# Performance work log

Hardware: AMD Instinct MI355X
Metric: run time of the kernel (lower is better)

The kernel has to match this reference:

```python
import jax, jax.numpy as jnp
import numpy as np
from jax import lax

NPOINTS = [1024, 256, 64, 16]
RADII = [0.02, 0.04, 0.06, 0.08]
NSAMPLE = [32, 32, 16, 16]
# per-level MLP widths; first entry already includes the +3 for use_xyz concat
MLPS = [[6, 32, 32, 64], [67, 64, 64, 128], [131, 128, 128, 256], [259, 256, 256, 512]]
EPS = 1e-5


def setup_inputs() -> dict:
    key = jax.random.key(0)
    B, N = 8, 16384
    pc = jax.random.uniform(jax.random.fold_in(key, 0), (B, N, 6), jnp.float32)
    # xyz into a 0.2-cube so the hard-coded radii (0.02..0.08) find real neighborhoods
    pc = pc.at[..., :3].multiply(0.2)
    inp = {"pointcloud": pc}
    ki = 1
    for l, m in enumerate(MLPS):
        for j in range(len(m) - 1):
            cin, cout = m[j], m[j + 1]
            inp[f"w{l}{j}"] = jax.random.normal(jax.random.fold_in(key, ki), (cin, cout), jnp.float32) * (1.0 / float(np.sqrt(cin)))
            inp[f"g{l}{j}"] = jnp.ones((cout,), jnp.float32)
            inp[f"b{l}{j}"] = jnp.zeros((cout,), jnp.float32)
            ki += 1
    return inp


def _fps(xyz, npoint):
    # iterative farthest point sampling, start at index 0 (matches CUDA kernel)
    B, N, _ = xyz.shape

    def step(carry, _):
        mind, last = carry
        lastp = jnp.take_along_axis(xyz, last[:, None, None], axis=1)  # [B,1,3]
        d = jnp.sum((xyz - lastp) ** 2, axis=-1)                       # [B,N]
        mind = jnp.minimum(mind, d)
        nxt = jnp.argmax(mind, axis=1).astype(jnp.int32)
        return (mind, nxt), last

    init = (jnp.full((B, N), 1e10, xyz.dtype), jnp.zeros((B,), jnp.int32))
    _, idx = lax.scan(step, init, None, length=npoint)
    return jnp.transpose(idx)  # [B,npoint]


def _gather(pts, idx):
    # pts [B,N,C], idx [B,...] -> [B,...,C]
    return jax.vmap(lambda p, i: p[i])(pts, idx)


def _ball_query(xyz, centers, radius, nsample):
    # first nsample points (in index order) within radius; pad with first hit (0 if none)
    N = xyz.shape[1]
    d2 = jnp.sum((centers[:, :, None, :] - xyz[:, None, :, :]) ** 2, axis=-1)  # [B,S,N]
    key = jnp.where(d2 < radius * radius, jnp.arange(N, dtype=jnp.int32), N)
    negtop, _ = lax.top_k(-key, nsample)
    sel = -negtop                      # ascending candidate indices
    valid = sel < N
    first = jnp.where(valid[..., :1], sel[..., :1], 0)
    return jnp.where(valid, sel, first)  # [B,S,nsample] int32


def _sa(xyz, feats, npoint, radius, nsample, layers):
    fps_idx = lax.stop_gradient(_fps(xyz, npoint))
    new_xyz = _gather(xyz, fps_idx)                    # [B,S,3]
    idx = _ball_query(xyz, new_xyz, radius, nsample)   # [B,S,K]
    g = _gather(xyz, idx) - new_xyz[:, :, None, :]     # centered grouped xyz [B,S,K,3]
    g = jnp.concatenate([g, _gather(feats, idx)], axis=-1)  # use_xyz concat -> [B,S,K,3+C]
    x = g
    for W, gamma, beta in layers:
        x = jnp.einsum('bski,io->bsko', x, W)          # 1x1 conv, bias=False (bn on)
        mu = jnp.mean(x, axis=(0, 1, 2))               # BN training-mode batch stats
        var = jnp.var(x, axis=(0, 1, 2))
        x = jax.nn.relu(gamma * (x - mu) * lax.rsqrt(var + EPS) + beta)
    return new_xyz, jnp.max(x, axis=2)                 # max-pool over neighbors -> [B,S,Cout]


def reference(pointcloud, w00, g00, b00, w01, g01, b01, w02, g02, b02,
              w10, g10, b10, w11, g11, b11, w12, g12, b12,
              w20, g20, b20, w21, g21, b21, w22, g22, b22,
              w30, g30, b30, w31, g31, b31, w32, g32, b32):
    params = [
        [(w00, g00, b00), (w01, g01, b01), (w02, g02, b02)],
        [(w10, g10, b10), (w11, g11, b11), (w12, g12, b12)],
        [(w20, g20, b20), (w21, g21, b21), (w22, g22, b22)],
        [(w30, g30, b30), (w31, g31, b31), (w32, g32, b32)],
    ]
    xyz = pointcloud[..., :3]
    feats = pointcloud[..., 3:]   # channels-last (torch keeps [B,C,N]; pure layout diff)
    l_xyz, l_feats = [xyz], [feats]
    for k in range(4):
        nx, nf = _sa(l_xyz[k], l_feats[k], NPOINTS[k], RADII[k], NSAMPLE[k], params[k])
        l_xyz.append(nx)
        l_feats.append(nf)
    return tuple(l_xyz) + tuple(l_feats)
```

## Files before the change

kernel.cpp:

```cpp
#include <hip/hip_runtime.h>

#define WAVE 64

__global__ __launch_bounds__(256) void split_kernel(const float* __restrict__ pc,
    float* __restrict__ xyz, float* __restrict__ feats, int total) {
  int t = blockIdx.x * blockDim.x + threadIdx.x;
  if (t >= total) return;
  const float* p = pc + (size_t)t * 6;
  xyz[t * 3 + 0] = p[0]; xyz[t * 3 + 1] = p[1]; xyz[t * 3 + 2] = p[2];
  feats[t * 3 + 0] = p[3]; feats[t * 3 + 1] = p[4]; feats[t * 3 + 2] = p[5];
}

__global__ __launch_bounds__(256) void zero_kernel(float* __restrict__ p, int n) {
  int t = blockIdx.x * blockDim.x + threadIdx.x;
  if (t < n) p[t] = 0.f;
}

__device__ __forceinline__ unsigned mapf(float f) {
  unsigned b = __float_as_uint(f);
  return (b & 0x80000000u) ? ~b : (b | 0x80000000u);
}
__device__ __forceinline__ float unmapf(unsigned u) {
  unsigned b = (u & 0x80000000u) ? (u ^ 0x80000000u) : ~u;
  return __uint_as_float(b);
}

__device__ __forceinline__ unsigned long long dpp_max_u64(unsigned long long v) {
#define DPP_STEP_U64(ctrl) { \
    unsigned lo_ = (unsigned)v, hi_ = (unsigned)(v >> 32); \
    unsigned tlo_ = (unsigned)__builtin_amdgcn_update_dpp((int)lo_, (int)lo_, ctrl, 0xf, 0xf, false); \
    unsigned thi_ = (unsigned)__builtin_amdgcn_update_dpp((int)hi_, (int)hi_, ctrl, 0xf, 0xf, false); \
    unsigned long long t_ = ((unsigned long long)thi_ << 32) | tlo_; \
    if (t_ > v) v = t_; }
  DPP_STEP_U64(0x111) DPP_STEP_U64(0x112) DPP_STEP_U64(0x114)
  DPP_STEP_U64(0x118) DPP_STEP_U64(0x142) DPP_STEP_U64(0x143)
#undef DPP_STEP_U64
  return v;
}

#define FPS_W   8
#define FPS_PT  8
__global__ __launch_bounds__(256, 4) void fps_big_multi_kernel(
    const float* __restrict__ xyz, float* __restrict__ new_xyz,
    unsigned long long* __restrict__ gkey, int N, int S) {
  const int b = blockIdx.x & 7;
  const int w = blockIdx.x >> 3;
  const int tid = threadIdx.x;
  const int lane = tid & 63;
  const int wv = tid >> 6;
  const float* px = xyz + (size_t)b * N * 3;
  const int base = w * (FPS_PT * 256);
  __shared__ unsigned long long s_cand[4];
  __shared__ unsigned long long s_win;
  float rx[FPS_PT], ry[FPS_PT], rz[FPS_PT], mind[FPS_PT];
#pragma unroll
  for (int p = 0; p < FPS_PT; ++p) {
    int i = base + p * 256 + tid;
    rx[p] = px[i * 3 + 0]; ry[p] = px[i * 3 + 1]; rz[p] = px[i * 3 + 2];
    asm volatile("" : "+v"(rx[p]), "+v"(ry[p]), "+v"(rz[p]));
    mind[p] = 1e10f;
  }
  float qx = px[0], qy = px[1], qz = px[2];
  if (w == 0 && tid == 0) {
    float* o = new_xyz + (size_t)b * S * 3;
    o[0] = qx; o[1] = qy; o[2] = qz;
  }
  unsigned long long* slots = gkey + (size_t)b * S * FPS_W;
  for (unsigned it = 1; it < (unsigned)S; ++it) {
    float bestv = -1.f; unsigned besti = 0;
#pragma unroll
    for (int p = 0; p < FPS_PT; ++p) {
      float dx = __fsub_rn(rx[p], qx);
      float dy = __fsub_rn(ry[p], qy);
      float dz = __fsub_rn(rz[p], qz);
      float d = __fadd_rn(__fadd_rn(__fmul_rn(dx, dx), __fmul_rn(dy, dy)), __fmul_rn(dz, dz));
      float mo = fminf(mind[p], d);
      mind[p] = mo;
      if (mo > bestv) { bestv = mo; besti = (unsigned)(base + p * 256 + tid); }
    }
    unsigned long long key = ((unsigned long long)__float_as_uint(bestv) << 32)
                           | (0xFFFFFFFFu - besti);
    key = dpp_max_u64(key);
    if (lane == 63) s_cand[wv] = key;
    __syncthreads();
    if (tid < 64) {
      unsigned long long k = s_cand[lane & 3];
#pragma unroll
      for (int off = 1; off < 4; off <<= 1) {
        unsigned long long o = __shfl_xor(k, off, 4);
        if (o > k) k = o;
      }
      if (lane == 0) {
        atomicExch(&slots[(size_t)it * FPS_W + w], k);
      }
      unsigned long long kk = 0ull;
      if (lane < FPS_W) {
        unsigned long long* sl = &slots[(size_t)it * FPS_W + lane];
        unsigned long long t0 = __builtin_amdgcn_s_memrealtime();
        int r = 0;
        for (;;) {
          kk = __hip_atomic_load(sl, __ATOMIC_RELAXED, __HIP_MEMORY_SCOPE_AGENT);
          if (kk) break;
          if (++r > 256) {
            kk = atomicMax(sl, 0ull);
            if (kk) break;
            if (__builtin_amdgcn_s_memrealtime() - t0 > 2000000ull) {
              kk = 0xFFFFFFFFull;
              break;
            }
            __builtin_amdgcn_s_sleep(1);
          }
        }
      }
#pragma unroll
      for (int off = 1; off < FPS_W; off <<= 1) {
        unsigned long long o = __shfl_xor(kk, off, FPS_W);
        if (o > kk) kk = o;
      }
      if (lane == 0) s_win = kk;
    }
    __syncthreads();
    unsigned long long k = s_win;
    int last = (int)((0xFFFFFFFFu - (unsigned)k) & 16383u);
    const float* q = px + (size_t)last * 3;
    qx = q[0]; qy = q[1]; qz = q[2];
    if (w == 0 && tid == 0) {
      float* o = new_xyz + ((size_t)b * S + it) * 3;
      o[0] = qx; o[1] = qy; o[2] = qz;
    }
  }
}

__global__ void fps_small_kernel(const float* __restrict__ xyz,
    float* __restrict__ new_xyz, int N, int S) {
  const int b = blockIdx.x;
  const int tid = threadIdx.x;
  const int lane = tid & 63;
  const int wv = tid >> 6;
  const int NW = N >> 6;
  const float* px = xyz + (size_t)b * N * 3;
  __shared__ float sx[1024], sy[1024], sz[1024];
  __shared__ unsigned long long s_cand[2][16];
  float x = px[tid * 3 + 0], y = px[tid * 3 + 1], z = px[tid * 3 + 2];
  sx[tid] = x; sy[tid] = y; sz[tid] = z;
  float mind = 1e10f;
  float qx = px[0], qy = px[1], qz = px[2];
  if (tid == 0) {
    float* o = new_xyz + (size_t)b * S * 3;
    o[0] = qx; o[1] = qy; o[2] = qz;
  }
  __syncthreads();
  for (unsigned it = 1; it < (unsigned)S; ++it) {
    float dx = __fsub_rn(x, qx);
    float dy = __fsub_rn(y, qy);
    float dz = __fsub_rn(z, qz);
    float d = __fadd_rn(__fadd_rn(__fmul_rn(dx, dx), __fmul_rn(dy, dy)), __fmul_rn(dz, dz));
    mind = fminf(mind, d);
    unsigned long long key = ((unsigned long long)__float_as_uint(mind) << 32)
                           | (0xFFFFFFFFu - (unsigned)tid);
    key = dpp_max_u64(key);
    if (lane == 63) s_cand[it & 1u][wv] = key;
    __syncthreads();
    unsigned long long k = (lane < NW) ? s_cand[it & 1u][lane] : 0ull;
    k = dpp_max_u64(k);
    unsigned klo = (unsigned)__builtin_amdgcn_readlane((int)(unsigned)k, 63);
    int last = (int)(0xFFFFFFFFu - klo);
    qx = sx[last]; qy = sy[last]; qz = sz[last];
    if (tid == 0) {
      float* o = new_xyz + ((size_t)b * S + it) * 3;
      o[0] = qx; o[1] = qy; o[2] = qz;
    }
  }
}

__global__ __launch_bounds__(256) void ballquery_kernel(const float* __restrict__ xyz,
    const float* __restrict__ centers, int* __restrict__ out_idx,
    int N, int S, int nsample, float r2) {
  int gw = (blockIdx.x * blockDim.x + threadIdx.x) >> 6;
  int lane = threadIdx.x & 63;
  int b = gw / S;
  int s = gw - b * S;
  const float* px = xyz + (size_t)b * N * 3;
  const float* cp = centers + ((size_t)b * S + s) * 3;
  float cx = cp[0], cy = cp[1], cz = cp[2];
  int* out = out_idx + ((size_t)b * S + s) * nsample;
  int cnt = 0;
  int firsti = 0;
  for (int base = 0; base < N; base += WAVE) {
    int i = base + lane;
    float dx = __fsub_rn(cx, px[i * 3 + 0]);
    float dy = __fsub_rn(cy, px[i * 3 + 1]);
    float dz = __fsub_rn(cz, px[i * 3 + 2]);
    float d = __fadd_rn(__fadd_rn(__fmul_rn(dx, dx), __fmul_rn(dy, dy)), __fmul_rn(dz, dz));
    bool hit = d < r2;
    unsigned long long m = __ballot(hit);
    if (hit) {
      int slot = cnt + __popcll(m & ((1ull << lane) - 1ull));
      if (slot < nsample) out[slot] = i;
    }
    if (cnt == 0 && m) firsti = base + __ffsll((unsigned long long)m) - 1;
    cnt += __popcll(m);
    if (cnt >= nsample) break;
  }
  for (int q = cnt + lane; q < nsample; q += WAVE) out[q] = firsti;
}

#define BM 64
#define BN 64
#define BK 16
__global__ __launch_bounds__(256) void mm_fused_kernel(const float* __restrict__ A,
    const float* __restrict__ W, float* __restrict__ Y,
    float* __restrict__ st_out, const float* __restrict__ st_in,
    const float* __restrict__ g_in, const float* __restrict__ b_in,
    int R, int C, int Co, float inv_n,
    const int* __restrict__ idx, const float* __restrict__ xyz,
    const float* __restrict__ feats, const float* __restrict__ centers,
    int N, int kshift, int sshift, int ci,
    unsigned* __restrict__ extmax, unsigned* __restrict__ extmin) {
  __shared__ float As[BK][BM + 4];
  __shared__ float Bs[BK][BN + 4];
  __shared__ float s_mu[260], s_rs[260], s_g[260], s_b[260];
  __shared__ float s_sum[BN], s_sq[BN];
  __shared__ int s_idx[BM];
  __shared__ unsigned s_mx[4][BN], s_mn[4][BN];
  int r0 = blockIdx.x * BM;
  int n0 = blockIdx.y * BN;
  int tid = threadIdx.x;
  int tx = tid & 15, ty = tid >> 4;
  if (st_in) {
    for (int c = tid; c < C; c += 256) {
      float mu = st_in[c] * inv_n;
      float var = st_in[512 + c] * inv_n - mu * mu;
      s_mu[c] = mu; s_rs[c] = rsqrtf(var + 1e-5f);
      s_g[c] = g_in[c]; s_b[c] = b_in[c];
    }
  }
  if (idx && tid < BM) s_idx[tid] = idx[r0 + tid];
  if (tid < BN) { s_sum[tid] = 0.f; s_sq[tid] = 0.f; }
  if (extmax) {
    for (int t2 = tid; t2 < 4 * BN; t2 += 256) {
      ((unsigned*)s_mx)[t2] = 0u;
      ((unsigned*)s_mn)[t2] = 0xFFFFFFFFu;
    }
  }
  __syncthreads();
  float acc[4][4] = {};
  for (int k0 = 0; k0 < C; k0 += BK) {
#pragma unroll
    for (int u = 0; u < 4; ++u) {
      int lin = tid + u * 256;
      int row = lin >> 4;
      int cc = lin & 15;
      int c = k0 + cc;
      float v = 0.f;
      if (c < C) {
        if (idx) {
          int r = r0 + row;
          int g = r >> kshift;
          int bb = g >> sshift;
          int j = s_idx[row];
          if (c < 3) v = __fsub_rn(xyz[((size_t)bb * N + j) * 3 + c],
                                   centers[(size_t)g * 3 + c]);
          else       v = feats[((size_t)bb * N + j) * ci + (c - 3)];
        } else {
          v = A[(size_t)(r0 + row) * C + c];
          if (st_in) {
            v = s_g[c] * ((v - s_mu[c]) * s_rs[c]) + s_b[c];
            v = v > 0.f ? v : 0.f;
          }
        }
      }
      As[cc][row] = v;
    }
#pragma unroll
    for (int u = 0; u < 4; ++u) {
      int lin = tid + u * 256;
      int kk = lin >> 6;
      int n = lin & 63;
      int c = k0 + kk;
      Bs[kk][n] = (c < C && (n0 + n) < Co) ? W[(size_t)c * Co + n0 + n] : 0.f;
    }
    __syncthreads();
#pragma unroll
    for (int kk = 0; kk < BK; ++kk) {
      float a0[4], b0[4];
#pragma unroll
      for (int i = 0; i < 4; ++i) a0[i] = As[kk][ty * 4 + i];
#pragma unroll
      for (int jj = 0; jj < 4; ++jj) b0[jj] = Bs[kk][tx * 4 + jj];
#pragma unroll
      for (int i = 0; i < 4; ++i)
#pragma unroll
        for (int jj = 0; jj < 4; ++jj)
          acc[i][jj] = fmaf(a0[i], b0[jj], acc[i][jj]);
    }
    __syncthreads();
  }
  if (!extmax) {
#pragma unroll
    for (int i = 0; i < 4; ++i) {
      int r = r0 + ty * 4 + i;
#pragma unroll
      for (int jj = 0; jj < 4; ++jj) {
        int n = n0 + tx * 4 + jj;
        if (n < Co) Y[(size_t)r * Co + n] = acc[i][jj];
      }
    }
  } else {
    int gi = (ty * 4) >> kshift;
#pragma unroll
    for (int jj = 0; jj < 4; ++jj) {
      float mx = acc[0][jj], mn = acc[0][jj];
#pragma unroll
      for (int i = 1; i < 4; ++i) {
        mx = fmaxf(mx, acc[i][jj]); mn = fminf(mn, acc[i][jj]);
      }
      atomicMax(&s_mx[gi][tx * 4 + jj], mapf(mx));
      atomicMin(&s_mn[gi][tx * 4 + jj], mapf(mn));
    }
  }
#pragma unroll
  for (int jj = 0; jj < 4; ++jj) {
    float cs = 0.f, cq = 0.f;
#pragma unroll
    for (int i = 0; i < 4; ++i) { float v = acc[i][jj]; cs += v; cq += v * v; }
    atomicAdd(&s_sum[tx * 4 + jj], cs);
    atomicAdd(&s_sq[tx * 4 + jj], cq);
  }
  __syncthreads();
  if (tid < BN) {
    int n = n0 + tid;
    if (n < Co) {
      atomicAdd(&st_out[n], s_sum[tid]);
      atomicAdd(&st_out[512 + n], s_sq[tid]);
    }
  }
  if (extmax) {
    int gpb = BM >> kshift;
    if (tid < gpb * BN) {
      int gi = tid >> 6;
      int n = tid & 63;
      if (n0 + n < Co) {
        size_t o = (size_t)((r0 >> kshift) + gi) * Co + n0 + n;
        extmax[o] = s_mx[gi][n];
        extmin[o] = s_mn[gi][n];
      }
    }
  }
}

__global__ __launch_bounds__(256) void norm_max_final_kernel(
    const unsigned* __restrict__ extmax, const unsigned* __restrict__ extmin,
    float* __restrict__ O, const float* __restrict__ st,
    const float* __restrict__ gamma, const float* __restrict__ beta,
    int total, int Co, float inv_n) {
  int t = blockIdx.x * blockDim.x + threadIdx.x;
  if (t >= total) return;
  int c = t & (Co - 1);
  float mu = st[c] * inv_n;
  float var = st[512 + c] * inv_n - mu * mu;
  float rs = rsqrtf(var + 1e-5f);
  float ga = gamma[c], be = beta[c];
  float y = (ga >= 0.f) ? unmapf(extmax[t]) : unmapf(extmin[t]);
  float v = ga * ((y - mu) * rs) + be;
  O[t] = v > 0.f ? v : 0.f;
}

extern "C" void kernel_launch(void* const* d_in, const int* in_sizes, int n_in,
                              void* d_out, int out_size, void* d_ws, size_t ws_size,
                              hipStream_t stream) {
  const float* pc = (const float*)d_in[0];
  float* out = (float*)d_out;
  char* wsb = (char*)d_ws;

  int* ballidx = (int*)wsb;
  float* stats = (float*)(wsb + ((size_t)1 << 20));
  unsigned long long* gkey = (unsigned long long*)(wsb + ((size_t)2 << 20));
  unsigned* extmax = (unsigned*)(wsb + ((size_t)3 << 20));
  unsigned* extmin = (unsigned*)(wsb + ((size_t)5 << 20));
  float* bufA = (float*)(wsb + ((size_t)8 << 20));
  float* bufB = (float*)(wsb + ((size_t)42 << 20));

  const int B = 8;
  static const int Ns[4] = {16384, 1024, 256, 64};
  static const int Ss[4] = {1024, 256, 64, 16};
  static const int Ks[4] = {32, 32, 16, 16};
  static const int Ksh[4] = {5, 5, 4, 4};
  static const int Ssh[4] = {10, 8, 6, 4};
  static const double Rr[4] = {0.02, 0.04, 0.06, 0.08};
  static const int Ci[4] = {3, 64, 128, 256};
  static const int mlp[4][4] = {{6,32,32,64},{67,64,64,128},{131,128,128,256},{259,256,256,512}};
  static const size_t ox[5] = {0, 393216, 417792, 423936, 425472};
  static const size_t of[5] = {425856, 819072, 1343360, 1605504, 1736576};

  split_kernel<<<(B * 16384 + 255) / 256, 256, 0, stream>>>(pc, out + ox[0], out + of[0], B * 16384);
  zero_kernel<<<(524288 + 255) / 256, 256, 0, stream>>>(stats, 524288);

  for (int l = 0; l < 4; ++l) {
    const float* xyz = out + ox[l];
    const float* fts = out + of[l];
    float* nxyz = out + ox[l + 1];
    const int N = Ns[l], S = Ss[l], K = Ks[l], ci = Ci[l];
    const float r2 = (float)(Rr[l] * Rr[l]);
    (void)K;

    if (l == 0) fps_big_multi_kernel<<<B * FPS_W, 256, 0, stream>>>(xyz, nxyz, gkey, N, S);
    else        fps_small_kernel<<<B, N, 0, stream>>>(xyz, nxyz, N, S);

    ballquery_kernel<<<(B * S) / 4, 256, 0, stream>>>(xyz, nxyz, ballidx, N, S, Ks[l], r2);

    const int R = B * S * Ks[l];
    const float inv_n = 1.0f / (float)R;
    float* X = bufA; float* Y = bufB;
    const float* prev_st = nullptr;
    const float* prev_g = nullptr;
    const float* prev_b = nullptr;
    for (int j = 0; j < 3; ++j) {
      const int cin = mlp[l][j], cout = mlp[l][j + 1];
      const float* Wt = (const float*)d_in[1 + (l * 3 + j) * 3 + 0];
      const float* Ga = (const float*)d_in[1 + (l * 3 + j) * 3 + 1];
      const float* Be = (const float*)d_in[1 + (l * 3 + j) * 3 + 2];
      float* st = stats + (size_t)(l * 3 + j) * 1024;
      const bool last = (j == 2);
      dim3 grid(R / 64, (cout + 63) / 64);
      mm_fused_kernel<<<grid, 256, 0, stream>>>(
          (j == 0) ? nullptr : X, Wt, last ? nullptr : Y, st,
          prev_st, prev_g, prev_b, R, cin, cout, inv_n,
          (j == 0) ? ballidx : nullptr, xyz, fts, nxyz,
          N, Ksh[l], Ssh[l], ci,
          last ? extmax : nullptr, last ? extmin : nullptr);
      if (!last) {
        prev_st = st; prev_g = Ga; prev_b = Be;
        float* tswap = X; X = Y; Y = tswap;
      } else {
        int G = B * S;
        int tot = G * cout;
        norm_max_final_kernel<<<(tot + 255) / 256, 256, 0, stream>>>(
            extmax, extmin, out + of[l + 1], st, Ga, Be, tot, cout, inv_n);
      }
    }
  }
}
```

Measured before the change: 2.388 ms.

## Fuse ball query into first MLP GEMM and chain small FPS levels

Merges the split and zero kernels into one init kernel. Runs the three small FPS levels in a single 1024-thread block kernel, launched after the big FPS. Drops the separate ball-query kernel and instead computes neighbour indices into shared memory inside the first fused GEMM of each level. Adds a partial-K path in the GEMM inner loop that skips zero-padded k steps. This removes launches and the global index buffer round trip. In exchange, ball query work is repeated for each column block of the first GEMM, and the chained FPS leaves idle waves in the smaller phases.

```diff
diff --git a/kernel.cpp b/kernel.cpp
--- a/kernel.cpp
+++ b/kernel.cpp
@@ -2,18 +2,16 @@
 
 #define WAVE 64
 
-__global__ __launch_bounds__(256) void split_kernel(const float* __restrict__ pc,
-    float* __restrict__ xyz, float* __restrict__ feats, int total) {
+__global__ __launch_bounds__(256) void init_kernel(const float* __restrict__ pc,
+    float* __restrict__ xyz, float* __restrict__ feats, float* __restrict__ zbase,
+    int nsplit, int nzero) {
   int t = blockIdx.x * blockDim.x + threadIdx.x;
-  if (t >= total) return;
-  const float* p = pc + (size_t)t * 6;
-  xyz[t * 3 + 0] = p[0]; xyz[t * 3 + 1] = p[1]; xyz[t * 3 + 2] = p[2];
-  feats[t * 3 + 0] = p[3]; feats[t * 3 + 1] = p[4]; feats[t * 3 + 2] = p[5];
-}
-
-__global__ __launch_bounds__(256) void zero_kernel(float* __restrict__ p, int n) {
-  int t = blockIdx.x * blockDim.x + threadIdx.x;
-  if (t < n) p[t] = 0.f;
+  if (t < nsplit) {
+    const float* p = pc + (size_t)t * 6;
+    xyz[t * 3 + 0] = p[0]; xyz[t * 3 + 1] = p[1]; xyz[t * 3 + 2] = p[2];
+    feats[t * 3 + 0] = p[3]; feats[t * 3 + 1] = p[4]; feats[t * 3 + 2] = p[5];
+  }
+  if (t < nzero) zbase[t] = 0.f;
 }
 
 __device__ __forceinline__ unsigned mapf(float f) {
@@ -131,78 +129,59 @@
   }
 }
 
-__global__ void fps_small_kernel(const float* __restrict__ xyz,
-    float* __restrict__ new_xyz, int N, int S) {
+__global__ __launch_bounds__(1024) void fps_chain_kernel(
+    const float* __restrict__ p1, float* __restrict__ p2,
+    float* __restrict__ p3, float* __restrict__ p4) {
   const int b = blockIdx.x;
   const int tid = threadIdx.x;
   const int lane = tid & 63;
   const int wv = tid >> 6;
-  const int NW = N >> 6;
-  const float* px = xyz + (size_t)b * N * 3;
   __shared__ float sx[1024], sy[1024], sz[1024];
   __shared__ unsigned long long s_cand[2][16];
-  float x = px[tid * 3 + 0], y = px[tid * 3 + 1], z = px[tid * 3 + 2];
-  sx[tid] = x; sy[tid] = y; sz[tid] = z;
-  float mind = 1e10f;
-  float qx = px[0], qy = px[1], qz = px[2];
-  if (tid == 0) {
-    float* o = new_xyz + (size_t)b * S * 3;
-    o[0] = qx; o[1] = qy; o[2] = qz;
-  }
-  __syncthreads();
-  for (unsigned it = 1; it < (unsigned)S; ++it) {
-    float dx = __fsub_rn(x, qx);
-    float dy = __fsub_rn(y, qy);
-    float dz = __fsub_rn(z, qz);
-    float d = __fadd_rn(__fadd_rn(__fmul_rn(dx, dx), __fmul_rn(dy, dy)), __fmul_rn(dz, dz));
-    mind = fminf(mind, d);
-    unsigned long long key = ((unsigned long long)__float_as_uint(mind) << 32)
-                           | (0xFFFFFFFFu - (unsigned)tid);
-    key = dpp_max_u64(key);
-    if (lane == 63) s_cand[it & 1u][wv] = key;
-    __syncthreads();
-    unsigned long long k = (lane < NW) ? s_cand[it & 1u][lane] : 0ull;
-    k = dpp_max_u64(k);
-    unsigned klo = (unsigned)__builtin_amdgcn_readlane((int)(unsigned)k, 63);
-    int last = (int)(0xFFFFFFFFu - klo);
-    qx = sx[last]; qy = sy[last]; qz = sz[last];
-    if (tid == 0) {
-      float* o = new_xyz + ((size_t)b * S + it) * 3;
-      o[0] = qx; o[1] = qy; o[2] = qz;
-    }
-  }
-}
-
-__global__ __launch_bounds__(256) void ballquery_kernel(const float* __restrict__ xyz,
-    const float* __restrict__ centers, int* __restrict__ out_idx,
-    int N, int S, int nsample, float r2) {
-  int gw = (blockIdx.x * blockDim.x + threadIdx.x) >> 6;
-  int lane = threadIdx.x & 63;
-  int b = gw / S;
-  int s = gw - b * S;
-  const float* px = xyz + (size_t)b * N * 3;
-  const float* cp = centers + ((size_t)b * S + s) * 3;
-  float cx = cp[0], cy = cp[1], cz = cp[2];
-  int* out = out_idx + ((size_t)b * S + s) * nsample;
-  int cnt = 0;
-  int firsti = 0;
-  for (int base = 0; base < N; base += WAVE) {
-    int i = base + lane;
-    float dx = __fsub_rn(cx, px[i * 3 + 0]);
-    float dy = __fsub_rn(cy, px[i * 3 + 1]);
-    float dz = __fsub_rn(cz, px[i * 3 + 2]);
-    float d = __fadd_rn(__fadd_rn(__fmul_rn(dx, dx), __fmul_rn(dy, dy)), __fmul_rn(dz, dz));
-    bool hit = d < r2;
-    unsigned long long m = __ballot(hit);
-    if (hit) {
-      int slot = cnt + __popcll(m & ((1ull << lane) - 1ull));
-      if (slot < nsample) out[slot] = i;
-    }
-    if (cnt == 0 && m) firsti = base + __ffsll((unsigned long long)m) - 1;
-    cnt += __popcll(m);
-    if (cnt >= nsample) break;
-  }
-  for (int q = cnt + lane; q < nsample; q += WAVE) out[q] = firsti;
+  const float* srcs[3]; float* dsts[3];
+  srcs[0] = p1; srcs[1] = p2; srcs[2] = p3;
+  dsts[0] = p2; dsts[1] = p3; dsts[2] = p4;
+  const int Np[3] = {1024, 256, 64};
+  const int Sp[3] = {256, 64, 16};
+  for (int ph = 0; ph < 3; ++ph) {
+    const int N = Np[ph], S = Sp[ph], NW = N >> 6;
+    const float* px = srcs[ph] + (size_t)b * N * 3;
+    float* dst = dsts[ph] + (size_t)b * S * 3;
+    float x = 0.f, y = 0.f, z = 0.f, mind = 1e10f;
+    if (tid < N) {
+      x = px[tid * 3 + 0]; y = px[tid * 3 + 1]; z = px[tid * 3 + 2];
+      sx[tid] = x; sy[tid] = y; sz[tid] = z;
+    }
+    float qx = px[0], qy = px[1], qz = px[2];
+    if (tid == 0) { dst[0] = qx; dst[1] = qy; dst[2] = qz; }
+    __syncthreads();
+    for (unsigned it = 1; it < (unsigned)S; ++it) {
+      if (wv < NW) {
+        float dx = __fsub_rn(x, qx);
+        float dy = __fsub_rn(y, qy);
+        float dz = __fsub_rn(z, qz);
+        float d = __fadd_rn(__fadd_rn(__fmul_rn(dx, dx), __fmul_rn(dy, dy)), __fmul_rn(dz, dz));
+        mind = fminf(mind, d);
+        unsigned long long key = ((unsigned long long)__float_as_uint(mind) << 32)
+                               | (0xFFFFFFFFu - (unsigned)tid);
+        key = dpp_max_u64(key);
+        if (lane == 63) s_cand[it & 1u][wv] = key;
+      }
+      __syncthreads();
+      if (wv < NW) {
+        unsigned long long k = (lane < NW) ? s_cand[it & 1u][lane] : 0ull;
+        k = dpp_max_u64(k);
+        unsigned klo = (unsigned)__builtin_amdgcn_readlane((int)(unsigned)k, 63);
+        int last = (int)(0xFFFFFFFFu - klo);
+        qx = sx[last]; qy = sy[last]; qz = sz[last];
+        if (tid == 0) {
+          float* o = dst + (size_t)it * 3;
+          o[0] = qx; o[1] = qy; o[2] = qz;
+        }
+      }
+    }
+    __syncthreads();
+  }
 }
 
 #define BM 64
@@ -213,9 +192,9 @@
     float* __restrict__ st_out, const float* __restrict__ st_in,
     const float* __restrict__ g_in, const float* __restrict__ b_in,
     int R, int C, int Co, float inv_n,
-    const int* __restrict__ idx, const float* __restrict__ xyz,
+    int gather, const float* __restrict__ xyz,
     const float* __restrict__ feats, const float* __restrict__ centers,
-    int N, int kshift, int sshift, int ci,
+    int N, int kshift, int sshift, int ci, float r2,
     unsigned* __restrict__ extmax, unsigned* __restrict__ extmin) {
   __shared__ float As[BK][BM + 4];
   __shared__ float Bs[BK][BN + 4];
@@ -235,7 +214,37 @@
       s_g[c] = g_in[c]; s_b[c] = b_in[c];
     }
   }
-  if (idx && tid < BM) s_idx[tid] = idx[r0 + tid];
+  if (gather) {
+    int wvq = tid >> 6, ln = tid & 63;
+    int gpb = BM >> kshift;
+    if (wvq < gpb) {
+      int G = (r0 >> kshift) + wvq;
+      int bb = G >> sshift;
+      const float* px = xyz + (size_t)bb * N * 3;
+      float cx = centers[(size_t)G * 3 + 0];
+      float cy = centers[(size_t)G * 3 + 1];
+      float cz = centers[(size_t)G * 3 + 2];
+      int Kn = 1 << kshift;
+      int cnt = 0, firsti = 0;
+      for (int bs = 0; bs < N; bs += WAVE) {
+        int i = bs + ln;
+        float dx = __fsub_rn(cx, px[i * 3 + 0]);
+        float dy = __fsub_rn(cy, px[i * 3 + 1]);
+        float dz = __fsub_rn(cz, px[i * 3 + 2]);
+        float d = __fadd_rn(__fadd_rn(__fmul_rn(dx, dx), __fmul_rn(dy, dy)), __fmul_rn(dz, dz));
+        bool hit = d < r2;
+        unsigned long long m = __ballot(hit);
+        if (hit) {
+          int slot = cnt + __popcll(m & ((1ull << ln) - 1ull));
+          if (slot < Kn) s_idx[(wvq << kshift) + slot] = i;
+        }
+        if (cnt == 0 && m) firsti = bs + __ffsll((unsigned long long)m) - 1;
+        cnt += __popcll(m);
+        if (cnt >= Kn) break;
+      }
+      for (int q = cnt + ln; q < Kn; q += WAVE) s_idx[(wvq << kshift) + q] = firsti;
+    }
+  }
   if (tid < BN) { s_sum[tid] = 0.f; s_sq[tid] = 0.f; }
   if (extmax) {
     for (int t2 = tid; t2 < 4 * BN; t2 += 256) {
@@ -254,7 +263,7 @@
       int c = k0 + cc;
       float v = 0.f;
       if (c < C) {
-        if (idx) {
+        if (gather) {
           int r = r0 + row;
           int g = r >> kshift;
           int bb = g >> sshift;
@@ -281,18 +290,34 @@
       Bs[kk][n] = (c < C && (n0 + n) < Co) ? W[(size_t)c * Co + n0 + n] : 0.f;
     }
     __syncthreads();
-#pragma unroll
-    for (int kk = 0; kk < BK; ++kk) {
-      float a0[4], b0[4];
-#pragma unroll
-      for (int i = 0; i < 4; ++i) a0[i] = As[kk][ty * 4 + i];
-#pragma unroll
-      for (int jj = 0; jj < 4; ++jj) b0[jj] = Bs[kk][tx * 4 + jj];
-#pragma unroll
-      for (int i = 0; i < 4; ++i)
-#pragma unroll
-        for (int jj = 0; jj < 4; ++jj)
-          acc[i][jj] = fmaf(a0[i], b0[jj], acc[i][jj]);
+    int kmax = C - k0; if (kmax > BK) kmax = BK;
+    if (kmax == BK) {
+#pragma unroll
+      for (int kk = 0; kk < BK; ++kk) {
+        float a0[4], b0[4];
+#pragma unroll
+        for (int i = 0; i < 4; ++i) a0[i] = As[kk][ty * 4 + i];
+#pragma unroll
+        for (int jj = 0; jj < 4; ++jj) b0[jj] = Bs[kk][tx * 4 + jj];
+#pragma unroll
+        for (int i = 0; i < 4; ++i)
+#pragma unroll
+          for (int jj = 0; jj < 4; ++jj)
+            acc[i][jj] = fmaf(a0[i], b0[jj], acc[i][jj]);
+      }
+    } else {
+      for (int kk = 0; kk < kmax; ++kk) {
+        float a0[4], b0[4];
+#pragma unroll
+        for (int i = 0; i < 4; ++i) a0[i] = As[kk][ty * 4 + i];
+#pragma unroll
+        for (int jj = 0; jj < 4; ++jj) b0[jj] = Bs[kk][tx * 4 + jj];
+#pragma unroll
+        for (int i = 0; i < 4; ++i)
+#pragma unroll
+          for (int jj = 0; jj < 4; ++jj)
+            acc[i][jj] = fmaf(a0[i], b0[jj], acc[i][jj]);
+      }
     }
     __syncthreads();
   }
@@ -373,7 +398,6 @@
   float* out = (float*)d_out;
   char* wsb = (char*)d_ws;
 
-  int* ballidx = (int*)wsb;
   float* stats = (float*)(wsb + ((size_t)1 << 20));
   unsigned long long* gkey = (unsigned long long*)(wsb + ((size_t)2 << 20));
   unsigned* extmax = (unsigned*)(wsb + ((size_t)3 << 20));
@@ -393,21 +417,18 @@
   static const size_t ox[5] = {0, 393216, 417792, 423936, 425472};
   static const size_t of[5] = {425856, 819072, 1343360, 1605504, 1736576};
 
-  split_kernel<<<(B * 16384 + 255) / 256, 256, 0, stream>>>(pc, out + ox[0], out + of[0], B * 16384);
-  zero_kernel<<<(524288 + 255) / 256, 256, 0, stream>>>(stats, 524288);
+  init_kernel<<<(524288 + 255) / 256, 256, 0, stream>>>(pc, out + ox[0], out + of[0],
+                                                        stats, B * 16384, 524288);
+  fps_big_multi_kernel<<<B * FPS_W, 256, 0, stream>>>(out + ox[0], out + ox[1], gkey,
+                                                      16384, 1024);
+  fps_chain_kernel<<<B, 1024, 0, stream>>>(out + ox[1], out + ox[2], out + ox[3], out + ox[4]);
 
   for (int l = 0; l < 4; ++l) {
     const float* xyz = out + ox[l];
     const float* fts = out + of[l];
     float* nxyz = out + ox[l + 1];
-    const int N = Ns[l], S = Ss[l], K = Ks[l], ci = Ci[l];
+    const int N = Ns[l], S = Ss[l], ci = Ci[l];
     const float r2 = (float)(Rr[l] * Rr[l]);
-    (void)K;
-
-    if (l == 0) fps_big_multi_kernel<<<B * FPS_W, 256, 0, stream>>>(xyz, nxyz, gkey, N, S);
-    else        fps_small_kernel<<<B, N, 0, stream>>>(xyz, nxyz, N, S);
-
-    ballquery_kernel<<<(B * S) / 4, 256, 0, stream>>>(xyz, nxyz, ballidx, N, S, Ks[l], r2);
 
     const int R = B * S * Ks[l];
     const float inv_n = 1.0f / (float)R;
@@ -426,8 +447,8 @@
       mm_fused_kernel<<<grid, 256, 0, stream>>>(
           (j == 0) ? nullptr : X, Wt, last ? nullptr : Y, st,
           prev_st, prev_g, prev_b, R, cin, cout, inv_n,
-          (j == 0) ? ballidx : nullptr, xyz, fts, nxyz,
-          N, Ksh[l], Ssh[l], ci,
+          (j == 0) ? 1 : 0, xyz, fts, nxyz,
+          N, Ksh[l], Ssh[l], ci, r2,
           last ? extmax : nullptr, last ? extmin : nullptr);
       if (!last) {
         prev_st = st; prev_g = Ga; prev_b = Be;
```

Measured after the change: 2.601 ms. +8.9%, slower.
